# Kernel optimization log

Hardware: AMD Instinct MI355X
Metric: run time of the kernel (lower is better)

The kernel has to match this reference:

```python
import jax, jax.numpy as jnp
import numpy as np

D_MODEL = 1024
N_HEADS = 16
D_K = D_MODEL // N_HEADS
CAUSAL = True


def setup_inputs() -> dict:
    key = jax.random.key(0)
    ks = jax.random.split(key, 11)
    B, S, D = 2, 2048, D_MODEL
    scale = 1.0 / np.sqrt(D)
    inp = {
        "in_Q": jax.random.normal(ks[0], (B, S, D), jnp.float32),
        "in_K": jax.random.normal(ks[1], (B, S, D), jnp.float32),
        "in_V": jax.random.normal(ks[2], (B, S, D), jnp.float32),
        # torch Linear params: weight [out, in], bias [out]
        "Wq": jax.random.normal(ks[3], (D, D), jnp.float32) * scale,
        "bq": jax.random.normal(ks[4], (D,), jnp.float32) * scale,
        "Wk": jax.random.normal(ks[5], (D, D), jnp.float32) * scale,
        "bk": jax.random.normal(ks[6], (D,), jnp.float32) * scale,
        "Wv": jax.random.normal(ks[7], (D, D), jnp.float32) * scale,
        "bv": jax.random.normal(ks[8], (D,), jnp.float32) * scale,
        "Wo": jax.random.normal(ks[9], (D, D), jnp.float32) * scale,
        "bo": jax.random.normal(ks[10], (D,), jnp.float32) * scale,
    }
    return inp


def reference(in_Q, in_K, in_V, Wq, bq, Wk, bk, Wv, bv, Wo, bo):
    B, S, D = in_Q.shape
    H, dk = N_HEADS, D_K
    # Linear projections (torch: x @ W.T + b)
    Q = in_Q @ Wq.T + bq
    K = in_K @ Wk.T + bk
    V = in_V @ Wv.T + bv
    # split heads: [B, S, D] -> [B, H, S, dk]
    Qh = Q.reshape(B, S, H, dk).transpose(0, 2, 1, 3)
    Kh = K.reshape(B, S, H, dk).transpose(0, 2, 1, 3)
    Vh = V.reshape(B, S, H, dk).transpose(0, 2, 1, 3)
    # scores [B, H, S, S]
    scores = jnp.einsum("bhqd,bhkd->bhqk", Qh, Kh) / jnp.sqrt(jnp.float32(dk))
    if CAUSAL:
        mask = jnp.tril(jnp.ones((S, S), dtype=bool))
        scores = jnp.where(mask, scores, -jnp.inf)
    attn = jax.nn.softmax(scores, axis=-1)
    out = jnp.einsum("bhqk,bhkd->bhqd", attn, Vh)
    Hcat = out.transpose(0, 2, 1, 3).reshape(B, S, D)
    return Hcat @ Wo.T + bo
```

## Files before the change

kernel.cpp:

```cpp
#include <hip/hip_runtime.h>
#include <hip/hip_bf16.h>
#include <math.h>

#define D_MODEL 1024
#define NHEADS  16
#define DK      64
#define SEQ     2048
#define BATCH   2
#define MROWS   4096
#define NQT     (SEQ/64)

typedef unsigned short ushort_t;
using short8 = __attribute__((ext_vector_type(8))) short;
using f32x4  = __attribute__((ext_vector_type(4))) float;

__device__ __forceinline__ ushort_t f2bf(float x) {
    unsigned u = __float_as_uint(x);
    u = (u + 0x7FFFu + ((u >> 16) & 1u)) >> 16;
    return (ushort_t)u;
}

__device__ __forceinline__ unsigned pk2(float a, float b) {
    __hip_bfloat162 h = __float22bfloat162_rn(float2{a, b});
    unsigned u;
    __builtin_memcpy(&u, &h, 4);
    return u;
}

__device__ __forceinline__ void gll16(const ushort_t* g, ushort_t* l) {
    __builtin_amdgcn_global_load_lds(
        (const __attribute__((address_space(1))) void*)(g),
        (__attribute__((address_space(3))) void*)(l), 16, 0, 0);
}

__global__ __launch_bounds__(256) void cvt_bf16(
    const float* s0, const float* s1, const float* s2, const float* s3,
    const float* s4, const float* s5, const float* s6,
    ushort_t* d0, ushort_t* d1, ushort_t* d2, ushort_t* d3,
    ushort_t* d4, ushort_t* d5, ushort_t* d6, int nIn, int nW)
{
    const float* s; ushort_t* d; int n;
    switch (blockIdx.y) {
        case 0: s = s0; d = d0; n = nIn; break;
        case 1: s = s1; d = d1; n = nIn; break;
        case 2: s = s2; d = d2; n = nIn; break;
        case 3: s = s3; d = d3; n = nW;  break;
        case 4: s = s4; d = d4; n = nW;  break;
        case 5: s = s5; d = d5; n = nW;  break;
        default: s = s6; d = d6; n = nW; break;
    }
    int i = (blockIdx.x * 256 + threadIdx.x) * 4;
    if (i < n) {
        float4 v = *(const float4*)&s[i];
        ushort4 o;
        o.x = f2bf(v.x); o.y = f2bf(v.y); o.z = f2bf(v.z); o.w = f2bf(v.w);
        *(ushort4*)&d[i] = o;
    }
}

struct GemmArgs { const ushort_t* A; const ushort_t* W; const float* bias;
                  void* C; int mode; float oscale; };

template<int MODE>
__device__ __forceinline__ void gemm_core(const GemmArgs& ga,
                                          ushort_t* As, ushort_t* Bs)
{
    constexpr bool SWP = (MODE != 1);
    const int tid  = threadIdx.x;
    const int w    = tid >> 6, lane = tid & 63;
    const int quad = lane >> 4, lx = lane & 15;
    const int mw = (w >> 1) * 64, nw = (w & 1) * 64;
    const int bm = blockIdx.x * 128, bn = blockIdx.y * 128;
    const int K = D_MODEL;

    f32x4 acc[4][4];
#pragma unroll
    for (int mt = 0; mt < 4; ++mt)
#pragma unroll
        for (int nt = 0; nt < 4; ++nt)
            acc[mt][nt] = (f32x4){0.f, 0.f, 0.f, 0.f};

    float4 b4[4];
    float  bfr[4];
#pragma unroll
    for (int nt = 0; nt < 4; ++nt) {
        if (SWP) b4[nt] = *(const float4*)&ga.bias[bn + nw + nt * 16 + quad * 4];
        else     bfr[nt] = ga.bias[bn + nw + nt * 16 + lx];
    }

    for (int k0 = 0; k0 < K; k0 += 64) {
        __syncthreads();
#pragma unroll
        for (int i = 0; i < 4; ++i) {
            int r0 = (w * 4 + i) * 8;
            int rl = r0 + (lane >> 3);
            int g  = (lane & 7) ^ (rl & 7);
            gll16(&ga.A[(size_t)(bm + rl) * K + k0 + g * 8], &As[r0 * 64]);
            gll16(&ga.W[(size_t)(bn + rl) * K + k0 + g * 8], &Bs[r0 * 64]);
        }
        __syncthreads();

#pragma unroll
        for (int ks = 0; ks < 2; ++ks) {
            short8 af[4], bf[4];
#pragma unroll
            for (int mt = 0; mt < 4; ++mt) {
                int r = mw + mt * 16 + lx;
                af[mt] = *(const short8*)&As[r * 64 + (((ks * 4 + quad) ^ (r & 7)) << 3)];
            }
#pragma unroll
            for (int nt = 0; nt < 4; ++nt) {
                int r = nw + nt * 16 + lx;
                bf[nt] = *(const short8*)&Bs[r * 64 + (((ks * 4 + quad) ^ (r & 7)) << 3)];
            }
#pragma unroll
            for (int mt = 0; mt < 4; ++mt)
#pragma unroll
                for (int nt = 0; nt < 4; ++nt)
                    acc[mt][nt] = SWP
                        ? __builtin_amdgcn_mfma_f32_16x16x32_bf16(bf[nt], af[mt], acc[mt][nt], 0, 0, 0)
                        : __builtin_amdgcn_mfma_f32_16x16x32_bf16(af[mt], bf[nt], acc[mt][nt], 0, 0, 0);
        }
    }

    if (MODE == 0) {
        ushort_t* C = (ushort_t*)ga.C;
        const float os = ga.oscale;
#pragma unroll
        for (int mt = 0; mt < 4; ++mt) {
            int m = bm + mw + mt * 16 + lx;
#pragma unroll
            for (int nt = 0; nt < 4; ++nt) {
                int n0 = bn + nw + nt * 16 + quad * 4;
                uint2 u;
                u.x = pk2((acc[mt][nt][0] + b4[nt].x) * os, (acc[mt][nt][1] + b4[nt].y) * os);
                u.y = pk2((acc[mt][nt][2] + b4[nt].z) * os, (acc[mt][nt][3] + b4[nt].w) * os);
                *(uint2*)&C[(size_t)m * D_MODEL + n0] = u;
            }
        }
    } else {
        ushort_t* C = (ushort_t*)ga.C;
#pragma unroll
        for (int mt = 0; mt < 4; ++mt)
#pragma unroll
            for (int nt = 0; nt < 4; ++nt) {
                int n = bn + nw + nt * 16 + lx;
                int d = n & 63, h = n >> 6;
                int m0 = bm + mw + mt * 16 + quad * 4;
                int b = m0 >> 11, s0 = m0 & 2047;
                uint2 u;
                u.x = pk2(acc[mt][nt][0] + bfr[nt], acc[mt][nt][1] + bfr[nt]);
                u.y = pk2(acc[mt][nt][2] + bfr[nt], acc[mt][nt][3] + bfr[nt]);
                *(uint2*)&C[((size_t)(b * NHEADS + h) * DK + d) * SEQ + s0] = u;
            }
    }
}

__global__ __launch_bounds__(256) void gemm_mfma(GemmArgs g0, GemmArgs g1, GemmArgs g2)
{
    __shared__ ushort_t As[128 * 64];
    __shared__ ushort_t Bs[128 * 64];
    GemmArgs ga = (blockIdx.z == 0) ? g0 : ((blockIdx.z == 1) ? g1 : g2);
    if (ga.mode == 0) gemm_core<0>(ga, As, Bs);
    else              gemm_core<1>(ga, As, Bs);
}

__global__ __launch_bounds__(256) void gemm_o(
    const ushort_t* __restrict__ A, const ushort_t* __restrict__ W,
    const float* __restrict__ bias, float* __restrict__ C)
{
    __shared__ ushort_t As[64 * 64];
    __shared__ ushort_t Bs[128 * 64];

    const int tid  = threadIdx.x;
    const int w    = tid >> 6, lane = tid & 63;
    const int quad = lane >> 4, lx = lane & 15;
    const int mw = (w >> 1) * 32, nw = (w & 1) * 64;
    const int bm = blockIdx.x * 64, bn = blockIdx.y * 128;
    const int K = D_MODEL;

    f32x4 acc[2][4];
#pragma unroll
    for (int mt = 0; mt < 2; ++mt)
#pragma unroll
        for (int nt = 0; nt < 4; ++nt)
            acc[mt][nt] = (f32x4){0.f, 0.f, 0.f, 0.f};

    float4 b4[4];
#pragma unroll
    for (int nt = 0; nt < 4; ++nt)
        b4[nt] = *(const float4*)&bias[bn + nw + nt * 16 + quad * 4];

    for (int k0 = 0; k0 < K; k0 += 64) {
        __syncthreads();
#pragma unroll
        for (int i = 0; i < 2; ++i) {
            int r0 = (i * 4 + w) * 8;
            int rl = r0 + (lane >> 3);
            int g  = (lane & 7) ^ (rl & 7);
            gll16(&A[(size_t)(bm + rl) * K + k0 + g * 8], &As[r0 * 64]);
        }
#pragma unroll
        for (int i = 0; i < 4; ++i) {
            int r0 = (i * 4 + w) * 8;
            int rl = r0 + (lane >> 3);
            int g  = (lane & 7) ^ (rl & 7);
            gll16(&W[(size_t)(bn + rl) * K + k0 + g * 8], &Bs[r0 * 64]);
        }
        __syncthreads();

#pragma unroll
        for (int ks = 0; ks < 2; ++ks) {
            short8 af[2], bf[4];
#pragma unroll
            for (int mt = 0; mt < 2; ++mt) {
                int r = mw + mt * 16 + lx;
                af[mt] = *(const short8*)&As[r * 64 + (((ks * 4 + quad) ^ (r & 7)) << 3)];
            }
#pragma unroll
            for (int nt = 0; nt < 4; ++nt) {
                int r = nw + nt * 16 + lx;
                bf[nt] = *(const short8*)&Bs[r * 64 + (((ks * 4 + quad) ^ (r & 7)) << 3)];
            }
#pragma unroll
            for (int mt = 0; mt < 2; ++mt)
#pragma unroll
                for (int nt = 0; nt < 4; ++nt)
                    acc[mt][nt] = __builtin_amdgcn_mfma_f32_16x16x32_bf16(
                        bf[nt], af[mt], acc[mt][nt], 0, 0, 0);
        }
    }

#pragma unroll
    for (int mt = 0; mt < 2; ++mt) {
        int m = bm + mw + mt * 16 + lx;
#pragma unroll
        for (int nt = 0; nt < 4; ++nt) {
            int n0 = bn + nw + nt * 16 + quad * 4;
            float4 v;
            v.x = acc[mt][nt][0] + b4[nt].x;
            v.y = acc[mt][nt][1] + b4[nt].y;
            v.z = acc[mt][nt][2] + b4[nt].z;
            v.w = acc[mt][nt][3] + b4[nt].w;
            *(float4*)&C[(size_t)m * D_MODEL + n0] = v;
        }
    }
}

__device__ __forceinline__ void flash_tile(
    int qt, const size_t qbase, const size_t vbase,
    const ushort_t* __restrict__ Qp, const ushort_t* __restrict__ Kp,
    const ushort_t* __restrict__ Vt, ushort_t* __restrict__ Hc,
    ushort_t* Ks0, ushort_t* Ks1, ushort_t* Vs0, ushort_t* Vs1,
    ushort_t (*Ps)[16 * 64])
{
    const int tid  = threadIdx.x;
    const int w    = tid >> 6, lane = tid & 63;
    const int quad = lane >> 4, lx = lane & 15;

    {
#pragma unroll
        for (int i = 0; i < 2; ++i) {
            int r0 = (w + i * 4) * 8;
            int rl = r0 + (lane >> 3);
            int g  = (lane & 7) ^ (rl & 7);
            gll16(&Kp[qbase + (size_t)rl * D_MODEL + g * 8], &Ks0[r0 * 64]);
            gll16(&Vt[vbase + (size_t)rl * SEQ + g * 8], &Vs0[r0 * 64]);
        }
    }

    short8 qf[2];
    {
        size_t ro = qbase + (size_t)(qt * 64 + w * 16 + lx) * D_MODEL + quad * 8;
        qf[0] = *(const short8*)&Qp[ro];
        qf[1] = *(const short8*)&Qp[ro + 32];
    }

    char* Pb = (char*)&Ps[w][0] + (lx << 7);
    const int hsw = (lx & 7) << 4;

    f32x4 O[4];
#pragma unroll
    for (int nt = 0; nt < 4; ++nt) O[nt] = (f32x4){0.f, 0.f, 0.f, 0.f};
    float mrow = -INFINITY, lrow = 0.f;
    const int qin = w * 16 + lx;

    for (int kt = 0; kt <= qt; ++kt) {
        ushort_t* Ks = (kt & 1) ? Ks1 : Ks0;
        ushort_t* Vs = (kt & 1) ? Vs1 : Vs0;

        asm volatile("s_waitcnt vmcnt(0)" ::: "memory");
        asm volatile("s_barrier" ::: "memory");

        if (kt < qt) {
            ushort_t* Kn = (kt & 1) ? Ks0 : Ks1;
            ushort_t* Vn = (kt & 1) ? Vs0 : Vs1;
#pragma unroll
            for (int i = 0; i < 2; ++i) {
                int r0 = (w + i * 4) * 8;
                int rl = r0 + (lane >> 3);
                int g  = (lane & 7) ^ (rl & 7);
                gll16(&Kp[qbase + (size_t)((kt + 1) * 64 + rl) * D_MODEL + g * 8], &Kn[r0 * 64]);
                gll16(&Vt[vbase + (size_t)rl * SEQ + (kt + 1) * 64 + g * 8], &Vn[r0 * 64]);
            }
        }

        f32x4 s[4];
        __builtin_amdgcn_s_setprio(1);
#pragma unroll
        for (int nt = 0; nt < 4; ++nt) {
            int r = nt * 16 + lx;
            short8 kf0 = *(const short8*)&Ks[r * 64 + ((quad ^ (r & 7)) << 3)];
            short8 kf1 = *(const short8*)&Ks[r * 64 + (((4 + quad) ^ (r & 7)) << 3)];
            f32x4 z = (f32x4){0.f, 0.f, 0.f, 0.f};
            z = __builtin_amdgcn_mfma_f32_16x16x32_bf16(kf0, qf[0], z, 0, 0, 0);
            z = __builtin_amdgcn_mfma_f32_16x16x32_bf16(kf1, qf[1], z, 0, 0, 0);
            s[nt] = z;
        }
        __builtin_amdgcn_s_setprio(0);

        if (kt == qt) {
#pragma unroll
            for (int nt = 0; nt < 4; ++nt)
#pragma unroll
                for (int r = 0; r < 4; ++r)
                    if ((nt * 16 + quad * 4 + r) > qin) s[nt][r] = -INFINITY;
        }

        float tm = -INFINITY;
#pragma unroll
        for (int nt = 0; nt < 4; ++nt)
#pragma unroll
            for (int r = 0; r < 4; ++r) tm = fmaxf(tm, s[nt][r]);
        tm = fmaxf(tm, __shfl_xor(tm, 16, 64));
        tm = fmaxf(tm, __shfl_xor(tm, 32, 64));
        if (__any(tm > mrow + 8.f)) {
            float mnew = fmaxf(mrow, tm);
            float alpha = __builtin_amdgcn_exp2f(mrow - mnew);
            mrow = mnew;
            lrow *= alpha;
#pragma unroll
            for (int nt = 0; nt < 4; ++nt)
#pragma unroll
                for (int r = 0; r < 4; ++r) O[nt][r] *= alpha;
        }
        float rs = 0.f;
#pragma unroll
        for (int nt = 0; nt < 4; ++nt)
#pragma unroll
            for (int r = 0; r < 4; ++r) {
                float p = __builtin_amdgcn_exp2f(s[nt][r] - mrow);
                s[nt][r] = p;
                rs += p;
            }
        rs += __shfl_xor(rs, 16, 64);
        rs += __shfl_xor(rs, 32, 64);
        lrow += rs;

#pragma unroll
        for (int nt = 0; nt < 4; ++nt) {
            uint2 u;
            u.x = pk2(s[nt][0], s[nt][1]);
            u.y = pk2(s[nt][2], s[nt][3]);
            *(uint2*)(Pb + ((nt * 32 + quad * 8) ^ hsw)) = u;
        }

        short8 pf0 = *(const short8*)(Pb + ((quad * 16) ^ hsw));
        short8 pf1 = *(const short8*)(Pb + ((64 + quad * 16) ^ hsw));

        __builtin_amdgcn_s_setprio(1);
#pragma unroll
        for (int nt = 0; nt < 4; ++nt) {
            int r = nt * 16 + lx;
            short8 vf0 = *(const short8*)&Vs[r * 64 + ((quad ^ (r & 7)) << 3)];
            short8 vf1 = *(const short8*)&Vs[r * 64 + (((4 + quad) ^ (r & 7)) << 3)];
            O[nt] = __builtin_amdgcn_mfma_f32_16x16x32_bf16(vf0, pf0, O[nt], 0, 0, 0);
            O[nt] = __builtin_amdgcn_mfma_f32_16x16x32_bf16(vf1, pf1, O[nt], 0, 0, 0);
        }
        __builtin_amdgcn_s_setprio(0);
    }

    {
        float invl = 1.f / lrow;
        size_t ro = qbase + (size_t)(qt * 64 + w * 16 + lx) * D_MODEL;
#pragma unroll
        for (int nt = 0; nt < 4; ++nt) {
            uint2 u;
            u.x = pk2(O[nt][0] * invl, O[nt][1] * invl);
            u.y = pk2(O[nt][2] * invl, O[nt][3] * invl);
            *(uint2*)&Hc[ro + nt * 16 + quad * 4] = u;
        }
    }
}

__global__ __launch_bounds__(256) void flash_mfma(
    const ushort_t* __restrict__ Qp, const ushort_t* __restrict__ Kp,
    const ushort_t* __restrict__ Vt, ushort_t* __restrict__ Hc)
{
    __shared__ ushort_t Ks0[64 * 64], Ks1[64 * 64];
    __shared__ ushort_t Vs0[64 * 64], Vs1[64 * 64];
    __shared__ __align__(16) ushort_t Ps[4][16 * 64];

    const int flat = blockIdx.x;
    const int c  = flat & 7;
    const int j  = flat >> 3;
    const int cu = j & 31;
    const int m  = j >> 5;
    const int bh = c + (m << 3);
    const int u  = (cu + ((m >> 1) << 3)) & 31;
    const int qt = (m & 1) ? (NQT - 1 - u) : u;
    const int b = bh >> 4, h = bh & 15;

    const size_t qbase = (size_t)(b * SEQ) * D_MODEL + h * DK;
    const size_t vbase = (size_t)bh * DK * SEQ;

    flash_tile(qt, qbase, vbase, Qp, Kp, Vt, Hc, Ks0, Ks1, Vs0, Vs1, Ps);
}

extern "C" void kernel_launch(void* const* d_in, const int* in_sizes, int n_in,
                              void* d_out, int out_size, void* d_ws, size_t ws_size,
                              hipStream_t stream) {
    const float* inQ = (const float*)d_in[0];
    const float* inK = (const float*)d_in[1];
    const float* inV = (const float*)d_in[2];
    const float* Wq  = (const float*)d_in[3];
    const float* bq  = (const float*)d_in[4];
    const float* Wk  = (const float*)d_in[5];
    const float* bk  = (const float*)d_in[6];
    const float* Wv  = (const float*)d_in[7];
    const float* bv  = (const float*)d_in[8];
    const float* Wo  = (const float*)d_in[9];
    const float* bo  = (const float*)d_in[10];
    float* out = (float*)d_out;

    const size_t NI = (size_t)MROWS * D_MODEL;
    const size_t NW = (size_t)D_MODEL * D_MODEL;
    ushort_t* ws  = (ushort_t*)d_ws;
    ushort_t* Qb  = ws;
    ushort_t* Kb  = Qb  + NI;
    ushort_t* Vb  = Kb  + NI;
    ushort_t* Wqb = Vb  + NI;
    ushort_t* Wkb = Wqb + NW;
    ushort_t* Wvb = Wkb + NW;
    ushort_t* Wob = Wvb + NW;
    ushort_t* Qp  = Wob + NW;
    ushort_t* Kp  = Qp  + NI;
    ushort_t* Vtg = Kp  + NI;
    ushort_t* Hc  = Vtg + NI;

    cvt_bf16<<<dim3(NI / 1024, 7), 256, 0, stream>>>(
        inQ, inK, inV, Wq, Wk, Wv, Wo,
        Qb, Kb, Vb, Wqb, Wkb, Wvb, Wob, (int)NI, (int)NW);

    const float qsc = 0.125f * 1.44269504088896340736f;
    GemmArgs aq{Qb, Wqb, bq, (void*)Qp, 0, qsc};
    GemmArgs ak{Kb, Wkb, bk, (void*)Kp, 0, 1.0f};
    GemmArgs av{Vb, Wvb, bv, (void*)Vtg, 1, 1.0f};
    gemm_mfma<<<dim3(MROWS / 128, D_MODEL / 128, 3), 256, 0, stream>>>(aq, ak, av);

    flash_mfma<<<dim3(NQT * BATCH * NHEADS), 256, 0, stream>>>(Qp, Kp, Vtg, Hc);

    gemm_o<<<dim3(MROWS / 64, D_MODEL / 128), 256, 0, stream>>>(Hc, Wob, bo, out);
}
```

Before: 215.8 us.

## Software-pipeline QK^T of the next key tile ahead of the current softmax

The flash attention loop is restructured so the score MFMAs for key tile i+1 are issued before the softmax and PV work of tile i. K tiles are prefetched two iterations ahead, while V tiles are still loaded one iteration ahead. The aim is to overlap matrix-core work with the exp and reduction arithmetic, and the max and sum reductions are rewritten as balanced trees to shorten dependency chains. In exchange, the extra score fragments raise register pressure, and the s_setprio hints around the QK MFMAs are removed.

```diff
diff --git a/kernel.cpp b/kernel.cpp
--- a/kernel.cpp
+++ b/kernel.cpp
@@ -258,15 +258,13 @@
     const int w    = tid >> 6, lane = tid & 63;
     const int quad = lane >> 4, lx = lane & 15;
 
-    {
-#pragma unroll
-        for (int i = 0; i < 2; ++i) {
-            int r0 = (w + i * 4) * 8;
-            int rl = r0 + (lane >> 3);
-            int g  = (lane & 7) ^ (rl & 7);
-            gll16(&Kp[qbase + (size_t)rl * D_MODEL + g * 8], &Ks0[r0 * 64]);
-            gll16(&Vt[vbase + (size_t)rl * SEQ + g * 8], &Vs0[r0 * 64]);
-        }
+#pragma unroll
+    for (int i = 0; i < 2; ++i) {
+        int r0 = (w + i * 4) * 8;
+        int rl = r0 + (lane >> 3);
+        int g  = (lane & 7) ^ (rl & 7);
+        gll16(&Kp[qbase + (size_t)rl * D_MODEL + g * 8], &Ks0[r0 * 64]);
+        gll16(&Vt[vbase + (size_t)rl * SEQ + g * 8], &Vs0[r0 * 64]);
     }
 
     short8 qf[2];
@@ -285,53 +283,75 @@
     float mrow = -INFINITY, lrow = 0.f;
     const int qin = w * 16 + lx;
 
-    for (int kt = 0; kt <= qt; ++kt) {
-        ushort_t* Ks = (kt & 1) ? Ks1 : Ks0;
-        ushort_t* Vs = (kt & 1) ? Vs1 : Vs0;
+    asm volatile("s_waitcnt vmcnt(0)" ::: "memory");
+    asm volatile("s_barrier" ::: "memory");
+
+    if (qt >= 1) {
+#pragma unroll
+        for (int i = 0; i < 2; ++i) {
+            int r0 = (w + i * 4) * 8;
+            int rl = r0 + (lane >> 3);
+            int g  = (lane & 7) ^ (rl & 7);
+            gll16(&Kp[qbase + (size_t)(64 + rl) * D_MODEL + g * 8], &Ks1[r0 * 64]);
+        }
+    }
+
+    f32x4 sp[4];
+#pragma unroll
+    for (int nt = 0; nt < 4; ++nt) {
+        int r = nt * 16 + lx;
+        short8 kf0 = *(const short8*)&Ks0[r * 64 + ((quad ^ (r & 7)) << 3)];
+        short8 kf1 = *(const short8*)&Ks0[r * 64 + (((4 + quad) ^ (r & 7)) << 3)];
+        f32x4 z = (f32x4){0.f, 0.f, 0.f, 0.f};
+        z = __builtin_amdgcn_mfma_f32_16x16x32_bf16(kf0, qf[0], z, 0, 0, 0);
+        z = __builtin_amdgcn_mfma_f32_16x16x32_bf16(kf1, qf[1], z, 0, 0, 0);
+        sp[nt] = z;
+    }
+
+    for (int i = 0; i <= qt; ++i) {
+        ushort_t* Kn = ((i + 1) & 1) ? Ks1 : Ks0;
+        ushort_t* Kf = (i & 1) ? Ks1 : Ks0;
+        ushort_t* Vs = (i & 1) ? Vs1 : Vs0;
+        ushort_t* Vn = ((i + 1) & 1) ? Vs1 : Vs0;
 
         asm volatile("s_waitcnt vmcnt(0)" ::: "memory");
         asm volatile("s_barrier" ::: "memory");
 
-        if (kt < qt) {
-            ushort_t* Kn = (kt & 1) ? Ks0 : Ks1;
-            ushort_t* Vn = (kt & 1) ? Vs0 : Vs1;
-#pragma unroll
-            for (int i = 0; i < 2; ++i) {
-                int r0 = (w + i * 4) * 8;
+        f32x4 sn[4];
+        if (i < qt) {
+#pragma unroll
+            for (int j = 0; j < 2; ++j) {
+                int r0 = (w + j * 4) * 8;
                 int rl = r0 + (lane >> 3);
                 int g  = (lane & 7) ^ (rl & 7);
-                gll16(&Kp[qbase + (size_t)((kt + 1) * 64 + rl) * D_MODEL + g * 8], &Kn[r0 * 64]);
-                gll16(&Vt[vbase + (size_t)rl * SEQ + (kt + 1) * 64 + g * 8], &Vn[r0 * 64]);
-            }
-        }
-
-        f32x4 s[4];
-        __builtin_amdgcn_s_setprio(1);
-#pragma unroll
-        for (int nt = 0; nt < 4; ++nt) {
-            int r = nt * 16 + lx;
-            short8 kf0 = *(const short8*)&Ks[r * 64 + ((quad ^ (r & 7)) << 3)];
-            short8 kf1 = *(const short8*)&Ks[r * 64 + (((4 + quad) ^ (r & 7)) << 3)];
-            f32x4 z = (f32x4){0.f, 0.f, 0.f, 0.f};
-            z = __builtin_amdgcn_mfma_f32_16x16x32_bf16(kf0, qf[0], z, 0, 0, 0);
-            z = __builtin_amdgcn_mfma_f32_16x16x32_bf16(kf1, qf[1], z, 0, 0, 0);
-            s[nt] = z;
-        }
-        __builtin_amdgcn_s_setprio(0);
-
-        if (kt == qt) {
+                if (i + 2 <= qt)
+                    gll16(&Kp[qbase + (size_t)((i + 2) * 64 + rl) * D_MODEL + g * 8], &Kf[r0 * 64]);
+                gll16(&Vt[vbase + (size_t)rl * SEQ + (i + 1) * 64 + g * 8], &Vn[r0 * 64]);
+            }
+#pragma unroll
+            for (int nt = 0; nt < 4; ++nt) {
+                int r = nt * 16 + lx;
+                short8 kf0 = *(const short8*)&Kn[r * 64 + ((quad ^ (r & 7)) << 3)];
+                short8 kf1 = *(const short8*)&Kn[r * 64 + (((4 + quad) ^ (r & 7)) << 3)];
+                f32x4 z = (f32x4){0.f, 0.f, 0.f, 0.f};
+                z = __builtin_amdgcn_mfma_f32_16x16x32_bf16(kf0, qf[0], z, 0, 0, 0);
+                z = __builtin_amdgcn_mfma_f32_16x16x32_bf16(kf1, qf[1], z, 0, 0, 0);
+                sn[nt] = z;
+            }
+        }
+
+        if (i == qt) {
 #pragma unroll
             for (int nt = 0; nt < 4; ++nt)
 #pragma unroll
                 for (int r = 0; r < 4; ++r)
-                    if ((nt * 16 + quad * 4 + r) > qin) s[nt][r] = -INFINITY;
-        }
-
-        float tm = -INFINITY;
-#pragma unroll
-        for (int nt = 0; nt < 4; ++nt)
-#pragma unroll
-            for (int r = 0; r < 4; ++r) tm = fmaxf(tm, s[nt][r]);
+                    if ((nt * 16 + quad * 4 + r) > qin) sp[nt][r] = -INFINITY;
+        }
+        float m0 = fmaxf(fmaxf(sp[0][0], sp[0][1]), fmaxf(sp[0][2], sp[0][3]));
+        float m1 = fmaxf(fmaxf(sp[1][0], sp[1][1]), fmaxf(sp[1][2], sp[1][3]));
+        float m2 = fmaxf(fmaxf(sp[2][0], sp[2][1]), fmaxf(sp[2][2], sp[2][3]));
+        float m3 = fmaxf(fmaxf(sp[3][0], sp[3][1]), fmaxf(sp[3][2], sp[3][3]));
+        float tm = fmaxf(fmaxf(m0, m1), fmaxf(m2, m3));
         tm = fmaxf(tm, __shfl_xor(tm, 16, 64));
         tm = fmaxf(tm, __shfl_xor(tm, 32, 64));
         if (__any(tm > mrow + 8.f)) {
@@ -344,15 +364,16 @@
 #pragma unroll
                 for (int r = 0; r < 4; ++r) O[nt][r] *= alpha;
         }
-        float rs = 0.f;
 #pragma unroll
         for (int nt = 0; nt < 4; ++nt)
 #pragma unroll
-            for (int r = 0; r < 4; ++r) {
-                float p = __builtin_amdgcn_exp2f(s[nt][r] - mrow);
-                s[nt][r] = p;
-                rs += p;
-            }
+            for (int r = 0; r < 4; ++r)
+                sp[nt][r] = __builtin_amdgcn_exp2f(sp[nt][r] - mrow);
+        float r0s = (sp[0][0] + sp[0][1]) + (sp[0][2] + sp[0][3]);
+        float r1s = (sp[1][0] + sp[1][1]) + (sp[1][2] + sp[1][3]);
+        float r2s = (sp[2][0] + sp[2][1]) + (sp[2][2] + sp[2][3]);
+        float r3s = (sp[3][0] + sp[3][1]) + (sp[3][2] + sp[3][3]);
+        float rs = (r0s + r1s) + (r2s + r3s);
         rs += __shfl_xor(rs, 16, 64);
         rs += __shfl_xor(rs, 32, 64);
         lrow += rs;
@@ -360,11 +381,10 @@
 #pragma unroll
         for (int nt = 0; nt < 4; ++nt) {
             uint2 u;
-            u.x = pk2(s[nt][0], s[nt][1]);
-            u.y = pk2(s[nt][2], s[nt][3]);
+            u.x = pk2(sp[nt][0], sp[nt][1]);
+            u.y = pk2(sp[nt][2], sp[nt][3]);
             *(uint2*)(Pb + ((nt * 32 + quad * 8) ^ hsw)) = u;
         }
-
         short8 pf0 = *(const short8*)(Pb + ((quad * 16) ^ hsw));
         short8 pf1 = *(const short8*)(Pb + ((64 + quad * 16) ^ hsw));
 
@@ -378,6 +398,11 @@
             O[nt] = __builtin_amdgcn_mfma_f32_16x16x32_bf16(vf1, pf1, O[nt], 0, 0, 0);
         }
         __builtin_amdgcn_s_setprio(0);
+
+        if (i < qt) {
+#pragma unroll
+            for (int nt = 0; nt < 4; ++nt) sp[nt] = sn[nt];
+        }
     }
 
     {
```

Result: no change. 219.0 us (+1.5%).

## Process 128 query rows per flash block to share K/V tiles

Applied to the files above, without the earlier changes.

Each flash-attention block now handles two 64-row query tiles, with each wave keeping two sets of Q fragments, accumulators and softmax state. Every K/V tile loaded into LDS is reused by both halves, which halves global and LDS traffic for K/V per query row. The block-to-tile mapping is rewritten for 16 query tiles per head and still pairs early and late tiles so causal work stays balanced. The cost is half as many blocks (512), more registers per wave and extra branching on the diagonal tile, so occupancy and load balance may suffer.

```diff
diff --git a/kernel.cpp b/kernel.cpp
--- a/kernel.cpp
+++ b/kernel.cpp
@@ -8,7 +8,7 @@
 #define SEQ     2048
 #define BATCH   2
 #define MROWS   4096
-#define NQT     (SEQ/64)
+#define NQT2    (SEQ/128)
 
 typedef unsigned short ushort_t;
 using short8 = __attribute__((ext_vector_type(8))) short;
@@ -257,42 +257,46 @@
     const int tid  = threadIdx.x;
     const int w    = tid >> 6, lane = tid & 63;
     const int quad = lane >> 4, lx = lane & 15;
-
+    const int ktlast = 2 * qt + 1;
+
+#pragma unroll
+    for (int i = 0; i < 2; ++i) {
+        int r0 = (w + i * 4) * 8;
+        int rl = r0 + (lane >> 3);
+        int g  = (lane & 7) ^ (rl & 7);
+        gll16(&Kp[qbase + (size_t)rl * D_MODEL + g * 8], &Ks0[r0 * 64]);
+        gll16(&Vt[vbase + (size_t)rl * SEQ + g * 8], &Vs0[r0 * 64]);
+    }
+
+    short8 qf0[2], qf1[2];
     {
-#pragma unroll
-        for (int i = 0; i < 2; ++i) {
-            int r0 = (w + i * 4) * 8;
-            int rl = r0 + (lane >> 3);
-            int g  = (lane & 7) ^ (rl & 7);
-            gll16(&Kp[qbase + (size_t)rl * D_MODEL + g * 8], &Ks0[r0 * 64]);
-            gll16(&Vt[vbase + (size_t)rl * SEQ + g * 8], &Vs0[r0 * 64]);
-        }
-    }
-
-    short8 qf[2];
-    {
-        size_t ro = qbase + (size_t)(qt * 64 + w * 16 + lx) * D_MODEL + quad * 8;
-        qf[0] = *(const short8*)&Qp[ro];
-        qf[1] = *(const short8*)&Qp[ro + 32];
+        size_t ro = qbase + (size_t)(qt * 128 + w * 16 + lx) * D_MODEL + quad * 8;
+        qf0[0] = *(const short8*)&Qp[ro];
+        qf0[1] = *(const short8*)&Qp[ro + 32];
+        qf1[0] = *(const short8*)&Qp[ro + (size_t)64 * D_MODEL];
+        qf1[1] = *(const short8*)&Qp[ro + (size_t)64 * D_MODEL + 32];
     }
 
     char* Pb = (char*)&Ps[w][0] + (lx << 7);
     const int hsw = (lx & 7) << 4;
 
-    f32x4 O[4];
-#pragma unroll
-    for (int nt = 0; nt < 4; ++nt) O[nt] = (f32x4){0.f, 0.f, 0.f, 0.f};
-    float mrow = -INFINITY, lrow = 0.f;
-    const int qin = w * 16 + lx;
-
-    for (int kt = 0; kt <= qt; ++kt) {
+    f32x4 O0[4], O1[4];
+#pragma unroll
+    for (int nt = 0; nt < 4; ++nt) {
+        O0[nt] = (f32x4){0.f, 0.f, 0.f, 0.f};
+        O1[nt] = (f32x4){0.f, 0.f, 0.f, 0.f};
+    }
+    float m0 = -INFINITY, l0 = 0.f, m1 = -INFINITY, l1 = 0.f;
+    const int qd = w * 16 + lx;
+
+    for (int kt = 0; kt <= ktlast; ++kt) {
         ushort_t* Ks = (kt & 1) ? Ks1 : Ks0;
         ushort_t* Vs = (kt & 1) ? Vs1 : Vs0;
 
         asm volatile("s_waitcnt vmcnt(0)" ::: "memory");
         asm volatile("s_barrier" ::: "memory");
 
-        if (kt < qt) {
+        if (kt < ktlast) {
             ushort_t* Kn = (kt & 1) ? Ks0 : Ks1;
             ushort_t* Vn = (kt & 1) ? Vs0 : Vs1;
 #pragma unroll
@@ -305,89 +309,184 @@
             }
         }
 
-        f32x4 s[4];
+        const bool a0 = (kt < ktlast);
+
+        f32x4 s0[4], s1[4];
         __builtin_amdgcn_s_setprio(1);
-#pragma unroll
-        for (int nt = 0; nt < 4; ++nt) {
-            int r = nt * 16 + lx;
-            short8 kf0 = *(const short8*)&Ks[r * 64 + ((quad ^ (r & 7)) << 3)];
-            short8 kf1 = *(const short8*)&Ks[r * 64 + (((4 + quad) ^ (r & 7)) << 3)];
-            f32x4 z = (f32x4){0.f, 0.f, 0.f, 0.f};
-            z = __builtin_amdgcn_mfma_f32_16x16x32_bf16(kf0, qf[0], z, 0, 0, 0);
-            z = __builtin_amdgcn_mfma_f32_16x16x32_bf16(kf1, qf[1], z, 0, 0, 0);
-            s[nt] = z;
+        if (a0) {
+#pragma unroll
+            for (int nt = 0; nt < 4; ++nt) {
+                int r = nt * 16 + lx;
+                short8 kf0 = *(const short8*)&Ks[r * 64 + ((quad ^ (r & 7)) << 3)];
+                short8 kf1 = *(const short8*)&Ks[r * 64 + (((4 + quad) ^ (r & 7)) << 3)];
+                f32x4 z = (f32x4){0.f, 0.f, 0.f, 0.f};
+                z = __builtin_amdgcn_mfma_f32_16x16x32_bf16(kf0, qf0[0], z, 0, 0, 0);
+                z = __builtin_amdgcn_mfma_f32_16x16x32_bf16(kf1, qf0[1], z, 0, 0, 0);
+                s0[nt] = z;
+                f32x4 y = (f32x4){0.f, 0.f, 0.f, 0.f};
+                y = __builtin_amdgcn_mfma_f32_16x16x32_bf16(kf0, qf1[0], y, 0, 0, 0);
+                y = __builtin_amdgcn_mfma_f32_16x16x32_bf16(kf1, qf1[1], y, 0, 0, 0);
+                s1[nt] = y;
+            }
+        } else {
+#pragma unroll
+            for (int nt = 0; nt < 4; ++nt) {
+                int r = nt * 16 + lx;
+                short8 kf0 = *(const short8*)&Ks[r * 64 + ((quad ^ (r & 7)) << 3)];
+                short8 kf1 = *(const short8*)&Ks[r * 64 + (((4 + quad) ^ (r & 7)) << 3)];
+                f32x4 y = (f32x4){0.f, 0.f, 0.f, 0.f};
+                y = __builtin_amdgcn_mfma_f32_16x16x32_bf16(kf0, qf1[0], y, 0, 0, 0);
+                y = __builtin_amdgcn_mfma_f32_16x16x32_bf16(kf1, qf1[1], y, 0, 0, 0);
+                s1[nt] = y;
+            }
         }
         __builtin_amdgcn_s_setprio(0);
 
-        if (kt == qt) {
+        if (a0 && kt == 2 * qt) {
 #pragma unroll
             for (int nt = 0; nt < 4; ++nt)
 #pragma unroll
                 for (int r = 0; r < 4; ++r)
-                    if ((nt * 16 + quad * 4 + r) > qin) s[nt][r] = -INFINITY;
-        }
-
-        float tm = -INFINITY;
-#pragma unroll
-        for (int nt = 0; nt < 4; ++nt)
-#pragma unroll
-            for (int r = 0; r < 4; ++r) tm = fmaxf(tm, s[nt][r]);
-        tm = fmaxf(tm, __shfl_xor(tm, 16, 64));
-        tm = fmaxf(tm, __shfl_xor(tm, 32, 64));
-        if (__any(tm > mrow + 8.f)) {
-            float mnew = fmaxf(mrow, tm);
-            float alpha = __builtin_amdgcn_exp2f(mrow - mnew);
-            mrow = mnew;
-            lrow *= alpha;
+                    if ((nt * 16 + quad * 4 + r) > qd) s0[nt][r] = -INFINITY;
+        }
+        if (kt == ktlast) {
 #pragma unroll
             for (int nt = 0; nt < 4; ++nt)
 #pragma unroll
-                for (int r = 0; r < 4; ++r) O[nt][r] *= alpha;
-        }
-        float rs = 0.f;
-#pragma unroll
-        for (int nt = 0; nt < 4; ++nt)
-#pragma unroll
-            for (int r = 0; r < 4; ++r) {
-                float p = __builtin_amdgcn_exp2f(s[nt][r] - mrow);
-                s[nt][r] = p;
-                rs += p;
-            }
-        rs += __shfl_xor(rs, 16, 64);
-        rs += __shfl_xor(rs, 32, 64);
-        lrow += rs;
-
+                for (int r = 0; r < 4; ++r)
+                    if ((nt * 16 + quad * 4 + r) > qd) s1[nt][r] = -INFINITY;
+        }
+
+        if (a0) {
+            float a = fmaxf(fmaxf(s0[0][0], s0[0][1]), fmaxf(s0[0][2], s0[0][3]));
+            float b = fmaxf(fmaxf(s0[1][0], s0[1][1]), fmaxf(s0[1][2], s0[1][3]));
+            float c = fmaxf(fmaxf(s0[2][0], s0[2][1]), fmaxf(s0[2][2], s0[2][3]));
+            float d = fmaxf(fmaxf(s0[3][0], s0[3][1]), fmaxf(s0[3][2], s0[3][3]));
+            float tm = fmaxf(fmaxf(a, b), fmaxf(c, d));
+            tm = fmaxf(tm, __shfl_xor(tm, 16, 64));
+            tm = fmaxf(tm, __shfl_xor(tm, 32, 64));
+            if (__any(tm > m0 + 8.f)) {
+                float mnew = fmaxf(m0, tm);
+                float alpha = __builtin_amdgcn_exp2f(m0 - mnew);
+                m0 = mnew;
+                l0 *= alpha;
+#pragma unroll
+                for (int nt = 0; nt < 4; ++nt)
+#pragma unroll
+                    for (int r = 0; r < 4; ++r) O0[nt][r] *= alpha;
+            }
+#pragma unroll
+            for (int nt = 0; nt < 4; ++nt)
+#pragma unroll
+                for (int r = 0; r < 4; ++r)
+                    s0[nt][r] = __builtin_amdgcn_exp2f(s0[nt][r] - m0);
+            float r0s = (s0[0][0] + s0[0][1]) + (s0[0][2] + s0[0][3]);
+            float r1s = (s0[1][0] + s0[1][1]) + (s0[1][2] + s0[1][3]);
+            float r2s = (s0[2][0] + s0[2][1]) + (s0[2][2] + s0[2][3]);
+            float r3s = (s0[3][0] + s0[3][1]) + (s0[3][2] + s0[3][3]);
+            float rs = (r0s + r1s) + (r2s + r3s);
+            rs += __shfl_xor(rs, 16, 64);
+            rs += __shfl_xor(rs, 32, 64);
+            l0 += rs;
+        }
+
+        {
+            float a = fmaxf(fmaxf(s1[0][0], s1[0][1]), fmaxf(s1[0][2], s1[0][3]));
+            float b = fmaxf(fmaxf(s1[1][0], s1[1][1]), fmaxf(s1[1][2], s1[1][3]));
+            float c = fmaxf(fmaxf(s1[2][0], s1[2][1]), fmaxf(s1[2][2], s1[2][3]));
+            float d = fmaxf(fmaxf(s1[3][0], s1[3][1]), fmaxf(s1[3][2], s1[3][3]));
+            float tm = fmaxf(fmaxf(a, b), fmaxf(c, d));
+            tm = fmaxf(tm, __shfl_xor(tm, 16, 64));
+            tm = fmaxf(tm, __shfl_xor(tm, 32, 64));
+            if (__any(tm > m1 + 8.f)) {
+                float mnew = fmaxf(m1, tm);
+                float alpha = __builtin_amdgcn_exp2f(m1 - mnew);
+                m1 = mnew;
+                l1 *= alpha;
+#pragma unroll
+                for (int nt = 0; nt < 4; ++nt)
+#pragma unroll
+                    for (int r = 0; r < 4; ++r) O1[nt][r] *= alpha;
+            }
+#pragma unroll
+            for (int nt = 0; nt < 4; ++nt)
+#pragma unroll
+                for (int r = 0; r < 4; ++r)
+                    s1[nt][r] = __builtin_amdgcn_exp2f(s1[nt][r] - m1);
+            float r0s = (s1[0][0] + s1[0][1]) + (s1[0][2] + s1[0][3]);
+            float r1s = (s1[1][0] + s1[1][1]) + (s1[1][2] + s1[1][3]);
+            float r2s = (s1[2][0] + s1[2][1]) + (s1[2][2] + s1[2][3]);
+            float r3s = (s1[3][0] + s1[3][1]) + (s1[3][2] + s1[3][3]);
+            float rs = (r0s + r1s) + (r2s + r3s);
+            rs += __shfl_xor(rs, 16, 64);
+            rs += __shfl_xor(rs, 32, 64);
+            l1 += rs;
+        }
+
+        short8 pf00, pf01, pf10, pf11;
+        if (a0) {
+#pragma unroll
+            for (int nt = 0; nt < 4; ++nt) {
+                uint2 u;
+                u.x = pk2(s0[nt][0], s0[nt][1]);
+                u.y = pk2(s0[nt][2], s0[nt][3]);
+                *(uint2*)(Pb + ((nt * 32 + quad * 8) ^ hsw)) = u;
+            }
+            pf00 = *(const short8*)(Pb + ((quad * 16) ^ hsw));
+            pf01 = *(const short8*)(Pb + ((64 + quad * 16) ^ hsw));
+        }
 #pragma unroll
         for (int nt = 0; nt < 4; ++nt) {
             uint2 u;
-            u.x = pk2(s[nt][0], s[nt][1]);
-            u.y = pk2(s[nt][2], s[nt][3]);
+            u.x = pk2(s1[nt][0], s1[nt][1]);
+            u.y = pk2(s1[nt][2], s1[nt][3]);
             *(uint2*)(Pb + ((nt * 32 + quad * 8) ^ hsw)) = u;
         }
-
-        short8 pf0 = *(const short8*)(Pb + ((quad * 16) ^ hsw));
-        short8 pf1 = *(const short8*)(Pb + ((64 + quad * 16) ^ hsw));
+        pf10 = *(const short8*)(Pb + ((quad * 16) ^ hsw));
+        pf11 = *(const short8*)(Pb + ((64 + quad * 16) ^ hsw));
 
         __builtin_amdgcn_s_setprio(1);
-#pragma unroll
-        for (int nt = 0; nt < 4; ++nt) {
-            int r = nt * 16 + lx;
-            short8 vf0 = *(const short8*)&Vs[r * 64 + ((quad ^ (r & 7)) << 3)];
-            short8 vf1 = *(const short8*)&Vs[r * 64 + (((4 + quad) ^ (r & 7)) << 3)];
-            O[nt] = __builtin_amdgcn_mfma_f32_16x16x32_bf16(vf0, pf0, O[nt], 0, 0, 0);
-            O[nt] = __builtin_amdgcn_mfma_f32_16x16x32_bf16(vf1, pf1, O[nt], 0, 0, 0);
+        if (a0) {
+#pragma unroll
+            for (int nt = 0; nt < 4; ++nt) {
+                int r = nt * 16 + lx;
+                short8 vf0 = *(const short8*)&Vs[r * 64 + ((quad ^ (r & 7)) << 3)];
+                short8 vf1 = *(const short8*)&Vs[r * 64 + (((4 + quad) ^ (r & 7)) << 3)];
+                O0[nt] = __builtin_amdgcn_mfma_f32_16x16x32_bf16(vf0, pf00, O0[nt], 0, 0, 0);
+                O0[nt] = __builtin_amdgcn_mfma_f32_16x16x32_bf16(vf1, pf01, O0[nt], 0, 0, 0);
+                O1[nt] = __builtin_amdgcn_mfma_f32_16x16x32_bf16(vf0, pf10, O1[nt], 0, 0, 0);
+                O1[nt] = __builtin_amdgcn_mfma_f32_16x16x32_bf16(vf1, pf11, O1[nt], 0, 0, 0);
+            }
+        } else {
+#pragma unroll
+            for (int nt = 0; nt < 4; ++nt) {
+                int r = nt * 16 + lx;
+                short8 vf0 = *(const short8*)&Vs[r * 64 + ((quad ^ (r & 7)) << 3)];
+                short8 vf1 = *(const short8*)&Vs[r * 64 + (((4 + quad) ^ (r & 7)) << 3)];
+                O1[nt] = __builtin_amdgcn_mfma_f32_16x16x32_bf16(vf0, pf10, O1[nt], 0, 0, 0);
+                O1[nt] = __builtin_amdgcn_mfma_f32_16x16x32_bf16(vf1, pf11, O1[nt], 0, 0, 0);
+            }
         }
         __builtin_amdgcn_s_setprio(0);
     }
 
     {
-        float invl = 1.f / lrow;
-        size_t ro = qbase + (size_t)(qt * 64 + w * 16 + lx) * D_MODEL;
+        float invl = 1.f / l0;
+        size_t ro = qbase + (size_t)(qt * 128 + w * 16 + lx) * D_MODEL;
 #pragma unroll
         for (int nt = 0; nt < 4; ++nt) {
             uint2 u;
-            u.x = pk2(O[nt][0] * invl, O[nt][1] * invl);
-            u.y = pk2(O[nt][2] * invl, O[nt][3] * invl);
+            u.x = pk2(O0[nt][0] * invl, O0[nt][1] * invl);
+            u.y = pk2(O0[nt][2] * invl, O0[nt][3] * invl);
+            *(uint2*)&Hc[ro + nt * 16 + quad * 4] = u;
+        }
+        invl = 1.f / l1;
+        ro += (size_t)64 * D_MODEL;
+#pragma unroll
+        for (int nt = 0; nt < 4; ++nt) {
+            uint2 u;
+            u.x = pk2(O1[nt][0] * invl, O1[nt][1] * invl);
+            u.y = pk2(O1[nt][2] * invl, O1[nt][3] * invl);
             *(uint2*)&Hc[ro + nt * 16 + quad * 4] = u;
         }
     }
@@ -406,9 +505,9 @@
     const int j  = flat >> 3;
     const int cu = j & 31;
     const int m  = j >> 5;
-    const int bh = c + (m << 3);
-    const int u  = (cu + ((m >> 1) << 3)) & 31;
-    const int qt = (m & 1) ? (NQT - 1 - u) : u;
+    const int bh = c + ((cu >> 3) << 3);
+    const int u  = cu & 7;
+    const int qt = m ? (NQT2 - 1 - u) : u;
     const int b = bh >> 4, h = bh & 15;
 
     const size_t qbase = (size_t)(b * SEQ) * D_MODEL + h * DK;
@@ -458,7 +557,7 @@
     GemmArgs av{Vb, Wvb, bv, (void*)Vtg, 1, 1.0f};
     gemm_mfma<<<dim3(MROWS / 128, D_MODEL / 128, 3), 256, 0, stream>>>(aq, ak, av);
 
-    flash_mfma<<<dim3(NQT * BATCH * NHEADS), 256, 0, stream>>>(Qp, Kp, Vtg, Hc);
+    flash_mfma<<<dim3(NQT2 * BATCH * NHEADS), 256, 0, stream>>>(Qp, Kp, Vtg, Hc);
 
     gemm_o<<<dim3(MROWS / 64, D_MODEL / 128), 256, 0, stream>>>(Hc, Wob, bo, out);
 }
```

New measurement: 224.8 us. 1.04x slower.

## Run flash attention with one wave per block handling all 64 query rows

Applied to the files above, without the earlier changes.

The flash attention kernel now uses a single 64-lane wave per block instead of four waves. That wave processes four 16-row query groups and keeps the K/V fragments for each key tile in registers, so every LDS read of K and V is reused four times. Double-buffered LDS is replaced by a single buffer that is reloaded after the fragments are read into registers, which removes the block barrier. In exchange, register pressure rises sharply (Q, O and K/V fragments for four groups), the global-load prefetch has less compute to overlap with, and each CU holds fewer waves per block.

```diff
diff --git a/kernel.cpp b/kernel.cpp
--- a/kernel.cpp
+++ b/kernel.cpp
@@ -247,159 +247,13 @@
     }
 }
 
-__device__ __forceinline__ void flash_tile(
-    int qt, const size_t qbase, const size_t vbase,
-    const ushort_t* __restrict__ Qp, const ushort_t* __restrict__ Kp,
-    const ushort_t* __restrict__ Vt, ushort_t* __restrict__ Hc,
-    ushort_t* Ks0, ushort_t* Ks1, ushort_t* Vs0, ushort_t* Vs1,
-    ushort_t (*Ps)[16 * 64])
-{
-    const int tid  = threadIdx.x;
-    const int w    = tid >> 6, lane = tid & 63;
-    const int quad = lane >> 4, lx = lane & 15;
-
-    {
-#pragma unroll
-        for (int i = 0; i < 2; ++i) {
-            int r0 = (w + i * 4) * 8;
-            int rl = r0 + (lane >> 3);
-            int g  = (lane & 7) ^ (rl & 7);
-            gll16(&Kp[qbase + (size_t)rl * D_MODEL + g * 8], &Ks0[r0 * 64]);
-            gll16(&Vt[vbase + (size_t)rl * SEQ + g * 8], &Vs0[r0 * 64]);
-        }
-    }
-
-    short8 qf[2];
-    {
-        size_t ro = qbase + (size_t)(qt * 64 + w * 16 + lx) * D_MODEL + quad * 8;
-        qf[0] = *(const short8*)&Qp[ro];
-        qf[1] = *(const short8*)&Qp[ro + 32];
-    }
-
-    char* Pb = (char*)&Ps[w][0] + (lx << 7);
-    const int hsw = (lx & 7) << 4;
-
-    f32x4 O[4];
-#pragma unroll
-    for (int nt = 0; nt < 4; ++nt) O[nt] = (f32x4){0.f, 0.f, 0.f, 0.f};
-    float mrow = -INFINITY, lrow = 0.f;
-    const int qin = w * 16 + lx;
-
-    for (int kt = 0; kt <= qt; ++kt) {
-        ushort_t* Ks = (kt & 1) ? Ks1 : Ks0;
-        ushort_t* Vs = (kt & 1) ? Vs1 : Vs0;
-
-        asm volatile("s_waitcnt vmcnt(0)" ::: "memory");
-        asm volatile("s_barrier" ::: "memory");
-
-        if (kt < qt) {
-            ushort_t* Kn = (kt & 1) ? Ks0 : Ks1;
-            ushort_t* Vn = (kt & 1) ? Vs0 : Vs1;
-#pragma unroll
-            for (int i = 0; i < 2; ++i) {
-                int r0 = (w + i * 4) * 8;
-                int rl = r0 + (lane >> 3);
-                int g  = (lane & 7) ^ (rl & 7);
-                gll16(&Kp[qbase + (size_t)((kt + 1) * 64 + rl) * D_MODEL + g * 8], &Kn[r0 * 64]);
-                gll16(&Vt[vbase + (size_t)rl * SEQ + (kt + 1) * 64 + g * 8], &Vn[r0 * 64]);
-            }
-        }
-
-        f32x4 s[4];
-        __builtin_amdgcn_s_setprio(1);
-#pragma unroll
-        for (int nt = 0; nt < 4; ++nt) {
-            int r = nt * 16 + lx;
-            short8 kf0 = *(const short8*)&Ks[r * 64 + ((quad ^ (r & 7)) << 3)];
-            short8 kf1 = *(const short8*)&Ks[r * 64 + (((4 + quad) ^ (r & 7)) << 3)];
-            f32x4 z = (f32x4){0.f, 0.f, 0.f, 0.f};
-            z = __builtin_amdgcn_mfma_f32_16x16x32_bf16(kf0, qf[0], z, 0, 0, 0);
-            z = __builtin_amdgcn_mfma_f32_16x16x32_bf16(kf1, qf[1], z, 0, 0, 0);
-            s[nt] = z;
-        }
-        __builtin_amdgcn_s_setprio(0);
-
-        if (kt == qt) {
-#pragma unroll
-            for (int nt = 0; nt < 4; ++nt)
-#pragma unroll
-                for (int r = 0; r < 4; ++r)
-                    if ((nt * 16 + quad * 4 + r) > qin) s[nt][r] = -INFINITY;
-        }
-
-        float tm = -INFINITY;
-#pragma unroll
-        for (int nt = 0; nt < 4; ++nt)
-#pragma unroll
-            for (int r = 0; r < 4; ++r) tm = fmaxf(tm, s[nt][r]);
-        tm = fmaxf(tm, __shfl_xor(tm, 16, 64));
-        tm = fmaxf(tm, __shfl_xor(tm, 32, 64));
-        if (__any(tm > mrow + 8.f)) {
-            float mnew = fmaxf(mrow, tm);
-            float alpha = __builtin_amdgcn_exp2f(mrow - mnew);
-            mrow = mnew;
-            lrow *= alpha;
-#pragma unroll
-            for (int nt = 0; nt < 4; ++nt)
-#pragma unroll
-                for (int r = 0; r < 4; ++r) O[nt][r] *= alpha;
-        }
-        float rs = 0.f;
-#pragma unroll
-        for (int nt = 0; nt < 4; ++nt)
-#pragma unroll
-            for (int r = 0; r < 4; ++r) {
-                float p = __builtin_amdgcn_exp2f(s[nt][r] - mrow);
-                s[nt][r] = p;
-                rs += p;
-            }
-        rs += __shfl_xor(rs, 16, 64);
-        rs += __shfl_xor(rs, 32, 64);
-        lrow += rs;
-
-#pragma unroll
-        for (int nt = 0; nt < 4; ++nt) {
-            uint2 u;
-            u.x = pk2(s[nt][0], s[nt][1]);
-            u.y = pk2(s[nt][2], s[nt][3]);
-            *(uint2*)(Pb + ((nt * 32 + quad * 8) ^ hsw)) = u;
-        }
-
-        short8 pf0 = *(const short8*)(Pb + ((quad * 16) ^ hsw));
-        short8 pf1 = *(const short8*)(Pb + ((64 + quad * 16) ^ hsw));
-
-        __builtin_amdgcn_s_setprio(1);
-#pragma unroll
-        for (int nt = 0; nt < 4; ++nt) {
-            int r = nt * 16 + lx;
-            short8 vf0 = *(const short8*)&Vs[r * 64 + ((quad ^ (r & 7)) << 3)];
-            short8 vf1 = *(const short8*)&Vs[r * 64 + (((4 + quad) ^ (r & 7)) << 3)];
-            O[nt] = __builtin_amdgcn_mfma_f32_16x16x32_bf16(vf0, pf0, O[nt], 0, 0, 0);
-            O[nt] = __builtin_amdgcn_mfma_f32_16x16x32_bf16(vf1, pf1, O[nt], 0, 0, 0);
-        }
-        __builtin_amdgcn_s_setprio(0);
-    }
-
-    {
-        float invl = 1.f / lrow;
-        size_t ro = qbase + (size_t)(qt * 64 + w * 16 + lx) * D_MODEL;
-#pragma unroll
-        for (int nt = 0; nt < 4; ++nt) {
-            uint2 u;
-            u.x = pk2(O[nt][0] * invl, O[nt][1] * invl);
-            u.y = pk2(O[nt][2] * invl, O[nt][3] * invl);
-            *(uint2*)&Hc[ro + nt * 16 + quad * 4] = u;
-        }
-    }
-}
-
-__global__ __launch_bounds__(256) void flash_mfma(
+__global__ __launch_bounds__(64) void flash_mfma(
     const ushort_t* __restrict__ Qp, const ushort_t* __restrict__ Kp,
     const ushort_t* __restrict__ Vt, ushort_t* __restrict__ Hc)
 {
-    __shared__ ushort_t Ks0[64 * 64], Ks1[64 * 64];
-    __shared__ ushort_t Vs0[64 * 64], Vs1[64 * 64];
-    __shared__ __align__(16) ushort_t Ps[4][16 * 64];
+    __shared__ ushort_t Ks[64 * 64];
+    __shared__ ushort_t Vs[64 * 64];
+    __shared__ __align__(16) ushort_t Ps[16 * 64];
 
     const int flat = blockIdx.x;
     const int c  = flat & 7;
@@ -414,7 +268,151 @@
     const size_t qbase = (size_t)(b * SEQ) * D_MODEL + h * DK;
     const size_t vbase = (size_t)bh * DK * SEQ;
 
-    flash_tile(qt, qbase, vbase, Qp, Kp, Vt, Hc, Ks0, Ks1, Vs0, Vs1, Ps);
+    const int lane = threadIdx.x;
+    const int quad = lane >> 4, lx = lane & 15;
+
+#pragma unroll
+    for (int i = 0; i < 8; ++i) {
+        int r0 = i * 8;
+        int rl = r0 + (lane >> 3);
+        int g  = (lane & 7) ^ (rl & 7);
+        gll16(&Kp[qbase + (size_t)rl * D_MODEL + g * 8], &Ks[r0 * 64]);
+        gll16(&Vt[vbase + (size_t)rl * SEQ + g * 8], &Vs[r0 * 64]);
+    }
+
+    short8 qf[4][2];
+#pragma unroll
+    for (int g = 0; g < 4; ++g) {
+        size_t ro = qbase + (size_t)(qt * 64 + g * 16 + lx) * D_MODEL + quad * 8;
+        qf[g][0] = *(const short8*)&Qp[ro];
+        qf[g][1] = *(const short8*)&Qp[ro + 32];
+    }
+
+    char* Pb = (char*)&Ps[0] + (lx << 7);
+    const int hsw = (lx & 7) << 4;
+
+    f32x4 O[4][4];
+#pragma unroll
+    for (int g = 0; g < 4; ++g)
+#pragma unroll
+        for (int nt = 0; nt < 4; ++nt)
+            O[g][nt] = (f32x4){0.f, 0.f, 0.f, 0.f};
+    float mg[4] = {-INFINITY, -INFINITY, -INFINITY, -INFINITY};
+    float lg[4] = {0.f, 0.f, 0.f, 0.f};
+
+    for (int kt = 0; kt <= qt; ++kt) {
+        asm volatile("s_waitcnt vmcnt(0)" ::: "memory");
+
+        short8 kf[4][2], vf[4][2];
+#pragma unroll
+        for (int nt = 0; nt < 4; ++nt) {
+            int r = nt * 16 + lx;
+            kf[nt][0] = *(const short8*)&Ks[r * 64 + ((quad ^ (r & 7)) << 3)];
+            kf[nt][1] = *(const short8*)&Ks[r * 64 + (((4 + quad) ^ (r & 7)) << 3)];
+            vf[nt][0] = *(const short8*)&Vs[r * 64 + ((quad ^ (r & 7)) << 3)];
+            vf[nt][1] = *(const short8*)&Vs[r * 64 + (((4 + quad) ^ (r & 7)) << 3)];
+        }
+        asm volatile("s_waitcnt lgkmcnt(0)" ::: "memory");
+        __builtin_amdgcn_sched_barrier(0);
+
+        if (kt < qt) {
+#pragma unroll
+            for (int i = 0; i < 8; ++i) {
+                int r0 = i * 8;
+                int rl = r0 + (lane >> 3);
+                int g2 = (lane & 7) ^ (rl & 7);
+                gll16(&Kp[qbase + (size_t)((kt + 1) * 64 + rl) * D_MODEL + g2 * 8], &Ks[r0 * 64]);
+                gll16(&Vt[vbase + (size_t)rl * SEQ + (kt + 1) * 64 + g2 * 8], &Vs[r0 * 64]);
+            }
+        }
+
+        const bool diag = (kt == qt);
+
+#pragma unroll
+        for (int g = 0; g < 4; ++g) {
+            f32x4 s[4];
+            __builtin_amdgcn_s_setprio(1);
+#pragma unroll
+            for (int nt = 0; nt < 4; ++nt) {
+                f32x4 z = (f32x4){0.f, 0.f, 0.f, 0.f};
+                z = __builtin_amdgcn_mfma_f32_16x16x32_bf16(kf[nt][0], qf[g][0], z, 0, 0, 0);
+                z = __builtin_amdgcn_mfma_f32_16x16x32_bf16(kf[nt][1], qf[g][1], z, 0, 0, 0);
+                s[nt] = z;
+            }
+            __builtin_amdgcn_s_setprio(0);
+
+            if (diag) {
+                const int qd = g * 16 + lx;
+#pragma unroll
+                for (int nt = 0; nt < 4; ++nt)
+#pragma unroll
+                    for (int r = 0; r < 4; ++r)
+                        if ((nt * 16 + quad * 4 + r) > qd) s[nt][r] = -INFINITY;
+            }
+
+            float a0 = fmaxf(fmaxf(s[0][0], s[0][1]), fmaxf(s[0][2], s[0][3]));
+            float a1 = fmaxf(fmaxf(s[1][0], s[1][1]), fmaxf(s[1][2], s[1][3]));
+            float a2 = fmaxf(fmaxf(s[2][0], s[2][1]), fmaxf(s[2][2], s[2][3]));
+            float a3 = fmaxf(fmaxf(s[3][0], s[3][1]), fmaxf(s[3][2], s[3][3]));
+            float tm = fmaxf(fmaxf(a0, a1), fmaxf(a2, a3));
+            tm = fmaxf(tm, __shfl_xor(tm, 16, 64));
+            tm = fmaxf(tm, __shfl_xor(tm, 32, 64));
+            if (__any(tm > mg[g] + 8.f)) {
+                float mnew = fmaxf(mg[g], tm);
+                float alpha = __builtin_amdgcn_exp2f(mg[g] - mnew);
+                mg[g] = mnew;
+                lg[g] *= alpha;
+#pragma unroll
+                for (int nt = 0; nt < 4; ++nt)
+#pragma unroll
+                    for (int r = 0; r < 4; ++r) O[g][nt][r] *= alpha;
+            }
+#pragma unroll
+            for (int nt = 0; nt < 4; ++nt)
+#pragma unroll
+                for (int r = 0; r < 4; ++r)
+                    s[nt][r] = __builtin_amdgcn_exp2f(s[nt][r] - mg[g]);
+            float r0s = (s[0][0] + s[0][1]) + (s[0][2] + s[0][3]);
+            float r1s = (s[1][0] + s[1][1]) + (s[1][2] + s[1][3]);
+            float r2s = (s[2][0] + s[2][1]) + (s[2][2] + s[2][3]);
+            float r3s = (s[3][0] + s[3][1]) + (s[3][2] + s[3][3]);
+            float rs = (r0s + r1s) + (r2s + r3s);
+            rs += __shfl_xor(rs, 16, 64);
+            rs += __shfl_xor(rs, 32, 64);
+            lg[g] += rs;
+
+#pragma unroll
+            for (int nt = 0; nt < 4; ++nt) {
+                uint2 pu;
+                pu.x = pk2(s[nt][0], s[nt][1]);
+                pu.y = pk2(s[nt][2], s[nt][3]);
+                *(uint2*)(Pb + ((nt * 32 + quad * 8) ^ hsw)) = pu;
+            }
+            short8 pf0 = *(const short8*)(Pb + ((quad * 16) ^ hsw));
+            short8 pf1 = *(const short8*)(Pb + ((64 + quad * 16) ^ hsw));
+
+            __builtin_amdgcn_s_setprio(1);
+#pragma unroll
+            for (int nt = 0; nt < 4; ++nt) {
+                O[g][nt] = __builtin_amdgcn_mfma_f32_16x16x32_bf16(vf[nt][0], pf0, O[g][nt], 0, 0, 0);
+                O[g][nt] = __builtin_amdgcn_mfma_f32_16x16x32_bf16(vf[nt][1], pf1, O[g][nt], 0, 0, 0);
+            }
+            __builtin_amdgcn_s_setprio(0);
+        }
+    }
+
+#pragma unroll
+    for (int g = 0; g < 4; ++g) {
+        float invl = 1.f / lg[g];
+        size_t ro = qbase + (size_t)(qt * 64 + g * 16 + lx) * D_MODEL;
+#pragma unroll
+        for (int nt = 0; nt < 4; ++nt) {
+            uint2 pu;
+            pu.x = pk2(O[g][nt][0] * invl, O[g][nt][1] * invl);
+            pu.y = pk2(O[g][nt][2] * invl, O[g][nt][3] * invl);
+            *(uint2*)&Hc[ro + nt * 16 + quad * 4] = pu;
+        }
+    }
 }
 
 extern "C" void kernel_launch(void* const* d_in, const int* in_sizes, int n_in,
@@ -458,7 +456,7 @@
     GemmArgs av{Vb, Wvb, bv, (void*)Vtg, 1, 1.0f};
     gemm_mfma<<<dim3(MROWS / 128, D_MODEL / 128, 3), 256, 0, stream>>>(aq, ak, av);
 
-    flash_mfma<<<dim3(NQT * BATCH * NHEADS), 256, 0, stream>>>(Qp, Kp, Vtg, Hc);
+    flash_mfma<<<dim3(NQT * BATCH * NHEADS), 64, 0, stream>>>(Qp, Kp, Vtg, Hc);
 
     gemm_o<<<dim3(MROWS / 64, D_MODEL / 128), 256, 0, stream>>>(Hc, Wob, bo, out);
 }
```

New measurement: 261.5 us. +21.1%, slower.
